# Performance work log

Hardware: AMD Instinct MI355X
Metric: run time of the kernel (lower is better)

Reference implementation:

```python
import jax, jax.numpy as jnp
import numpy as np

G = 128          # voxel grid extent: (range_max - range_min) / voxel_size
N = 100_000      # occupied input voxels (pre-unique)
CIN, COUT = 32, 64
BN_EPS = 1e-5


def _build_positions():
    rng = np.random.default_rng(0)
    pos = rng.integers(0, G, size=(N, 3), dtype=np.int32)
    pos = np.unique(pos, axis=0)  # one feature row per active voxel
    # calculate_grid: offsets (i-2) for i in 0..2 -> {-2,-1,0}^3, filter to [0,G), unique
    offs = np.stack(np.meshgrid(*([np.arange(-2, 1)] * 3), indexing='ij'), -1).reshape(-1, 3)
    op = (pos[:, None, :] + offs[None, :, :]).reshape(-1, 3)
    op = op[(op.min(1) >= 0) & (op.max(1) < G)]
    op = np.unique(op, axis=0)
    return pos.astype(np.int32), op.astype(np.int32)


def setup_inputs() -> dict:
    pos, out_pos = _build_positions()
    key = jax.random.key(0)
    kf, kw = jax.random.split(key)
    n_in = pos.shape[0]
    features = jax.random.normal(kf, (n_in, CIN), dtype=jnp.float32)
    # kaiming-style fan-in init for the 3x3x3 kernel: fan_in = 27 * CIN
    weight = jax.random.normal(kw, (27, CIN, COUT), dtype=jnp.float32) * np.float32(np.sqrt(2.0 / (27 * CIN)))
    gamma = jnp.ones((COUT,), jnp.float32)
    beta = jnp.zeros((COUT,), jnp.float32)
    return {"features": features, "weight": weight, "gamma": gamma, "beta": beta,
            "positions": jnp.asarray(pos), "out_positions": jnp.asarray(out_pos)}


def reference(features, weight, gamma, beta, positions, out_positions):
    n_in, cin = features.shape
    cout = weight.shape[-1]
    # dense coord -> row-index hash grid; pad by 2 since taps reach out_pos + 2
    grid = jnp.full((G + 2, G + 2, G + 2), -1, jnp.int32)
    grid = grid.at[positions[:, 0], positions[:, 1], positions[:, 2]].set(
        jnp.arange(n_in, dtype=jnp.int32))
    # row of zeros for missing neighbors (index -1 wraps to the last row)
    feat_pad = jnp.concatenate([features, jnp.zeros((1, cin), features.dtype)], axis=0)
    ox, oy, oz = out_positions[:, 0], out_positions[:, 1], out_positions[:, 2]
    out = jnp.zeros((out_positions.shape[0], cout), features.dtype)
    k = 0
    # out position o gathers inputs at o + {0,1,2}^3 (mirror of the {-2,-1,0} offsets)
    for dx in range(3):
        for dy in range(3):
            for dz in range(3):
                idx = grid[ox + dx, oy + dy, oz + dz]          # [M] (-1 if empty)
                out = out + feat_pad[idx] @ weight[k]          # [M,Cin]@[Cin,Cout]
                k += 1
    # BatchNorm1d (training mode, stats over all output voxels) + ReLU
    mean = out.mean(axis=0)
    var = out.var(axis=0)
    out = (out - mean) * jax.lax.rsqrt(var + BN_EPS) * gamma + beta
    return jax.nn.relu(out)
```

## Files before the change

kernel.cpp:

```cpp
#include <hip/hip_runtime.h>

#define GD 130
#define GD2 (GD*GD)
#define GRID_ELEMS (GD*GD*GD)
#define STATS_BYTES 1024
#define WPB 16
#define CONV_BLOCKS 256
#define MAX_NIN 100000
#define MAX_NOUT 1600000
#define WSTRIDE 5

typedef _Float16 f16x8 __attribute__((ext_vector_type(8)));
typedef float    f32x16 __attribute__((ext_vector_type(16)));

__device__ _Float16 g_feat16[(MAX_NIN + 1) * 32];
__device__ _Float16 g_out16[(size_t)MAX_NOUT * 64];

__device__ __forceinline__ f32x16 mfma_f16(uint4 a, uint4 b, f32x16 c) {
    union { uint4 u; f16x8 h; } A, B;
    A.u = a; B.u = b;
    return __builtin_amdgcn_mfma_f32_32x32x16_f16(A.h, B.h, c, 0, 0, 0);
}

__global__ __launch_bounds__(256) void scatter_grid_k(
    const int* __restrict__ pos, int* __restrict__ grid, int n_in)
{
    int i = blockIdx.x * blockDim.x + threadIdx.x;
    if (i < n_in) {
        int x = pos[3*i], y = pos[3*i+1], z = pos[3*i+2];
        grid[(x*GD + y)*GD + z] = i;
    }
}

__global__ __launch_bounds__(256) void feat_to_f16_k(
    const float* __restrict__ feat, int n_in)
{
    int i = (blockIdx.x * blockDim.x + threadIdx.x) * 8;
    const int ntot = (n_in + 1) * 32;
    if (i < ntot) {
        union { _Float16 h[8]; uint4 u; } t;
        if (i < n_in * 32) {
            const float4 a = *reinterpret_cast<const float4*>(feat + i);
            const float4 b = *reinterpret_cast<const float4*>(feat + i + 4);
            t.h[0] = (_Float16)a.x; t.h[1] = (_Float16)a.y;
            t.h[2] = (_Float16)a.z; t.h[3] = (_Float16)a.w;
            t.h[4] = (_Float16)b.x; t.h[5] = (_Float16)b.y;
            t.h[6] = (_Float16)b.z; t.h[7] = (_Float16)b.w;
        } else {
            t.u = uint4{0u, 0u, 0u, 0u};
        }
        *reinterpret_cast<uint4*>(g_feat16 + i) = t.u;
    }
}

__device__ __forceinline__ int4 probe4(const int* __restrict__ grid, int base) {
    int4 p;
    __builtin_memcpy(&p, grid + base, 16);
    return p;
}

__device__ __forceinline__ int sel3(int4 p, int dz) {
    return dz == 0 ? p.x : (dz == 1 ? p.y : p.z);
}

__global__ __launch_bounds__(1024) void conv_mfma_k(
    const float* __restrict__ W,
    const int* __restrict__ outpos, const int* __restrict__ grid,
    float* __restrict__ stats, int n_out, int n_in)
{
    __shared__ uint4 wlds[27*64*WSTRIDE];
    __shared__ float sstat[128];

    const int tid  = threadIdx.x;
    const int lane = tid & 63;
    const int wid  = tid >> 6;
    const int oc   = lane & 31;
    const int hi   = lane >> 5;

    for (int g = tid; g < 27*64*4; g += 1024) {
        const int k   = g >> 8;
        const int rem = g & 255;
        const int o   = rem >> 2;
        const int q   = rem & 3;
        union { _Float16 h[8]; uint4 u; } t;
        #pragma unroll
        for (int j = 0; j < 8; ++j)
            t.h[j] = (_Float16)W[k*2048 + (q*8 + j)*64 + o];
        wlds[(k*64 + o)*WSTRIDE + q] = t.u;
    }
    if (tid < 128) sstat[tid] = 0.f;
    __syncthreads();

    unsigned* g_o32 = reinterpret_cast<unsigned*>(g_out16);

    const int nchunks = (n_out + 63) >> 6;
    const int xcd  = blockIdx.x & 7;
    const int lw   = (blockIdx.x >> 3) * WPB + wid;
    const int nlw  = (gridDim.x >> 3) * WPB;
    const int Q    = (nchunks + 7) >> 3;
    const int cLo  = xcd * Q;
    const int cHi  = min(cLo + Q, nchunks);

    float ssum0 = 0.f, ssq0 = 0.f, ssum1 = 0.f, ssq1 = 0.f;

    for (int ch = cLo + lw; ch < cHi; ch += nlw) {
        const int r0 = ch << 6;
        const int rb0 = min(r0 + oc,      n_out - 1);
        const int rb1 = min(r0 + 32 + oc, n_out - 1);
        int3 c0, c1;
        __builtin_memcpy(&c0, outpos + 3*rb0, 12);
        __builtin_memcpy(&c1, outpos + 3*rb1, 12);
        const int gb0 = (c0.x*GD + c0.y)*GD + c0.z;
        const int gb1 = (c1.x*GD + c1.y)*GD + c1.z;

        f32x16 acc00 = {0.f};
        f32x16 acc01 = {0.f};
        f32x16 acc10 = {0.f};
        f32x16 acc11 = {0.f};

        #pragma unroll
        for (int g = 0; g < 9; ++g) {
            const int off = (g/3)*GD2 + (g%3)*GD;
            const int4 p0 = probe4(grid, gb0 + off);
            const int4 p1 = probe4(grid, gb1 + off);
            #pragma unroll
            for (int dz = 0; dz < 3; ++dz) {
                const int t = g*3 + dz;
                const int wb = (t*64 + oc)*WSTRIDE + hi;
                const uint4 b00 = wlds[wb];
                const uint4 b10 = wlds[wb + 2];
                const uint4 b01 = wlds[wb + 32*WSTRIDE];
                const uint4 b11 = wlds[wb + 32*WSTRIDE + 2];
                const int i0 = sel3(p0, dz);
                const int i1 = sel3(p1, dz);
                const int s0 = i0 < 0 ? n_in : i0;
                const int s1 = i1 < 0 ? n_in : i1;
                const uint4* fp0 = reinterpret_cast<const uint4*>(
                    g_feat16 + (size_t)s0 * 32);
                const uint4* fp1 = reinterpret_cast<const uint4*>(
                    g_feat16 + (size_t)s1 * 32);
                const uint4 a00 = fp0[hi], a01 = fp0[2 + hi];
                const uint4 a10 = fp1[hi], a11 = fp1[2 + hi];
                acc00 = mfma_f16(a00, b00, acc00);
                acc00 = mfma_f16(a01, b10, acc00);
                acc01 = mfma_f16(a00, b01, acc01);
                acc01 = mfma_f16(a01, b11, acc01);
                acc10 = mfma_f16(a10, b00, acc10);
                acc10 = mfma_f16(a11, b10, acc10);
                acc11 = mfma_f16(a10, b01, acc11);
                acc11 = mfma_f16(a11, b11, acc11);
            }
        }

        if (r0 + 64 <= n_out) {
            #pragma unroll
            for (int j = 0; j < 16; ++j) {
                const int rl = (j & 3) + 8*(j >> 2) + 4*hi;
                union { unsigned u; _Float16 h[2]; } q0, q1;
                const float v00 = acc00[j], v01 = acc01[j];
                const float v10 = acc10[j], v11 = acc11[j];
                q0.h[0] = (_Float16)v00; q0.h[1] = (_Float16)v01;
                q1.h[0] = (_Float16)v10; q1.h[1] = (_Float16)v11;
                g_o32[(size_t)(r0 + rl) * 32 + oc]      = q0.u;
                g_o32[(size_t)(r0 + 32 + rl) * 32 + oc] = q1.u;
                ssum0 += v00 + v10; ssq0 = fmaf(v00, v00, fmaf(v10, v10, ssq0));
                ssum1 += v01 + v11; ssq1 = fmaf(v01, v01, fmaf(v11, v11, ssq1));
            }
        } else {
            #pragma unroll
            for (int j = 0; j < 16; ++j) {
                const int rl = (j & 3) + 8*(j >> 2) + 4*hi;
                if (r0 + rl < n_out) {
                    const float v00 = acc00[j], v01 = acc01[j];
                    union { unsigned u; _Float16 h[2]; } q0;
                    q0.h[0] = (_Float16)v00; q0.h[1] = (_Float16)v01;
                    g_o32[(size_t)(r0 + rl) * 32 + oc] = q0.u;
                    ssum0 += v00; ssq0 = fmaf(v00, v00, ssq0);
                    ssum1 += v01; ssq1 = fmaf(v01, v01, ssq1);
                }
                if (r0 + 32 + rl < n_out) {
                    const float v10 = acc10[j], v11 = acc11[j];
                    union { unsigned u; _Float16 h[2]; } q1;
                    q1.h[0] = (_Float16)v10; q1.h[1] = (_Float16)v11;
                    g_o32[(size_t)(r0 + 32 + rl) * 32 + oc] = q1.u;
                    ssum0 += v10; ssq0 = fmaf(v10, v10, ssq0);
                    ssum1 += v11; ssq1 = fmaf(v11, v11, ssq1);
                }
            }
        }
    }

    atomicAdd(&sstat[oc],          ssum0);
    atomicAdd(&sstat[32 + oc],     ssum1);
    atomicAdd(&sstat[64 + oc],     ssq0);
    atomicAdd(&sstat[96 + oc],     ssq1);
    __syncthreads();
    if (tid < 128) unsafeAtomicAdd(&stats[tid], sstat[tid]);
}

__global__ __launch_bounds__(256) void bn_relu_k(
    float* __restrict__ out, const float* __restrict__ stats,
    const float* __restrict__ gamma, const float* __restrict__ beta, int n_out)
{
    __shared__ float sc[64], sh[64];
    if (threadIdx.x < 64) {
        const int c = threadIdx.x;
        const double inv_n = 1.0 / (double)n_out;
        const double mean = (double)stats[c] * inv_n;
        const double var  = (double)stats[64 + c] * inv_n - mean * mean;
        const float scale = gamma[c] * rsqrtf((float)var + 1e-5f);
        sc[c] = scale;
        sh[c] = beta[c] - (float)mean * scale;
    }
    __syncthreads();

    const size_t total8 = (size_t)n_out * 8;
    for (size_t t = (size_t)blockIdx.x * blockDim.x + threadIdx.x;
         t < total8; t += (size_t)gridDim.x * blockDim.x) {
        union { uint4 u; _Float16 h[8]; } v;
        v.u = *reinterpret_cast<const uint4*>(g_out16 + t * 8);
        const int c0 = ((int)(t & 7)) * 4;
        float4 r0, r1;
        r0.x = fmaxf(fmaf((float)v.h[0], sc[c0+0],    sh[c0+0]),    0.f);
        r1.x = fmaxf(fmaf((float)v.h[1], sc[c0+32],   sh[c0+32]),   0.f);
        r0.y = fmaxf(fmaf((float)v.h[2], sc[c0+1],    sh[c0+1]),    0.f);
        r1.y = fmaxf(fmaf((float)v.h[3], sc[c0+33],   sh[c0+33]),   0.f);
        r0.z = fmaxf(fmaf((float)v.h[4], sc[c0+2],    sh[c0+2]),    0.f);
        r1.z = fmaxf(fmaf((float)v.h[5], sc[c0+34],   sh[c0+34]),   0.f);
        r0.w = fmaxf(fmaf((float)v.h[6], sc[c0+3],    sh[c0+3]),    0.f);
        r1.w = fmaxf(fmaf((float)v.h[7], sc[c0+35],   sh[c0+35]),   0.f);
        float* rowp = out + (size_t)(t >> 3) * 64;
        *reinterpret_cast<float4*>(rowp + c0)      = r0;
        *reinterpret_cast<float4*>(rowp + 32 + c0) = r1;
    }
}

extern "C" void kernel_launch(void* const* d_in, const int* in_sizes, int n_in_arrs,
                              void* d_out, int out_size, void* d_ws, size_t ws_size,
                              hipStream_t stream)
{
    const float* feat   = (const float*)d_in[0];
    const float* W      = (const float*)d_in[1];
    const float* gamma  = (const float*)d_in[2];
    const float* beta   = (const float*)d_in[3];
    const int*   pos    = (const int*)d_in[4];
    const int*   outpos = (const int*)d_in[5];

    const int n_in  = in_sizes[0] / 32;
    const int n_out = in_sizes[5] / 3;

    float* out   = (float*)d_out;
    float* stats = (float*)d_ws;
    int*   grid  = (int*)((char*)d_ws + STATS_BYTES);

    hipMemsetAsync(stats, 0, STATS_BYTES, stream);
    hipMemsetAsync(grid, 0xFF, ((size_t)GRID_ELEMS + 4) * 4, stream);

    scatter_grid_k<<<(n_in + 255) / 256, 256, 0, stream>>>(pos, grid, n_in);
    feat_to_f16_k<<<((n_in + 1) * 4 + 255) / 256, 256, 0, stream>>>(feat, n_in);
    conv_mfma_k<<<CONV_BLOCKS, 1024, 0, stream>>>(W, outpos, grid, stats, n_out, n_in);
    bn_relu_k<<<2048, 256, 0, stream>>>(out, stats, gamma, beta, n_out);
}
```

Before: 369.0 us.

## Pre-convert weights to f16 in global memory and read them via cache instead of LDS

Adds a small kernel that converts the 27x32x64 weights to f16 once into a global buffer. The conv kernel drops its per-block LDS weight staging and instead loads the weight fragments straight from global memory, relying on the L1/L2 caches. This removes each block's redundant conversion prologue and the large LDS allocation, which frees occupancy, and the block count is doubled to use it. In exchange, every MFMA step now issues global/cache loads for weights where it used to read LDS, which may add latency in the inner loop.

```diff
diff --git a/kernel.cpp b/kernel.cpp
--- a/kernel.cpp
+++ b/kernel.cpp
@@ -5,16 +5,16 @@
 #define GRID_ELEMS (GD*GD*GD)
 #define STATS_BYTES 1024
 #define WPB 16
-#define CONV_BLOCKS 256
+#define CONV_BLOCKS 512
 #define MAX_NIN 100000
 #define MAX_NOUT 1600000
-#define WSTRIDE 5
 
 typedef _Float16 f16x8 __attribute__((ext_vector_type(8)));
 typedef float    f32x16 __attribute__((ext_vector_type(16)));
 
 __device__ _Float16 g_feat16[(MAX_NIN + 1) * 32];
 __device__ _Float16 g_out16[(size_t)MAX_NOUT * 64];
+__device__ uint4    g_w16[27 * 4 * 64];
 
 __device__ __forceinline__ f32x16 mfma_f16(uint4 a, uint4 b, f32x16 c) {
     union { uint4 u; f16x8 h; } A, B;
@@ -53,6 +53,21 @@
     }
 }
 
+__global__ __launch_bounds__(256) void w_to_f16_k(const float* __restrict__ W)
+{
+    int g = blockIdx.x * blockDim.x + threadIdx.x;
+    if (g < 27*4*64) {
+        const int k  = g >> 8;
+        const int kc = (g >> 6) & 3;
+        const int o  = g & 63;
+        union { _Float16 h[8]; uint4 u; } t;
+        #pragma unroll
+        for (int j = 0; j < 8; ++j)
+            t.h[j] = (_Float16)W[k*2048 + (kc*8 + j)*64 + o];
+        g_w16[g] = t.u;
+    }
+}
+
 __device__ __forceinline__ int4 probe4(const int* __restrict__ grid, int base) {
     int4 p;
     __builtin_memcpy(&p, grid + base, 16);
@@ -64,11 +79,9 @@
 }
 
 __global__ __launch_bounds__(1024) void conv_mfma_k(
-    const float* __restrict__ W,
     const int* __restrict__ outpos, const int* __restrict__ grid,
     float* __restrict__ stats, int n_out, int n_in)
 {
-    __shared__ uint4 wlds[27*64*WSTRIDE];
     __shared__ float sstat[128];
 
     const int tid  = threadIdx.x;
@@ -77,17 +90,6 @@
     const int oc   = lane & 31;
     const int hi   = lane >> 5;
 
-    for (int g = tid; g < 27*64*4; g += 1024) {
-        const int k   = g >> 8;
-        const int rem = g & 255;
-        const int o   = rem >> 2;
-        const int q   = rem & 3;
-        union { _Float16 h[8]; uint4 u; } t;
-        #pragma unroll
-        for (int j = 0; j < 8; ++j)
-            t.h[j] = (_Float16)W[k*2048 + (q*8 + j)*64 + o];
-        wlds[(k*64 + o)*WSTRIDE + q] = t.u;
-    }
     if (tid < 128) sstat[tid] = 0.f;
     __syncthreads();
 
@@ -126,11 +128,11 @@
             #pragma unroll
             for (int dz = 0; dz < 3; ++dz) {
                 const int t = g*3 + dz;
-                const int wb = (t*64 + oc)*WSTRIDE + hi;
-                const uint4 b00 = wlds[wb];
-                const uint4 b10 = wlds[wb + 2];
-                const uint4 b01 = wlds[wb + 32*WSTRIDE];
-                const uint4 b11 = wlds[wb + 32*WSTRIDE + 2];
+                const uint4* wt = g_w16 + t*256;
+                const uint4 b00 = wt[hi*64        + oc];
+                const uint4 b10 = wt[(2 + hi)*64  + oc];
+                const uint4 b01 = wt[hi*64        + 32 + oc];
+                const uint4 b11 = wt[(2 + hi)*64  + 32 + oc];
                 const int i0 = sel3(p0, dz);
                 const int i1 = sel3(p1, dz);
                 const int s0 = i0 < 0 ? n_in : i0;
@@ -258,6 +260,7 @@
 
     scatter_grid_k<<<(n_in + 255) / 256, 256, 0, stream>>>(pos, grid, n_in);
     feat_to_f16_k<<<((n_in + 1) * 4 + 255) / 256, 256, 0, stream>>>(feat, n_in);
-    conv_mfma_k<<<CONV_BLOCKS, 1024, 0, stream>>>(W, outpos, grid, stats, n_out, n_in);
+    w_to_f16_k<<<(27*4*64 + 255) / 256, 256, 0, stream>>>(W);
+    conv_mfma_k<<<CONV_BLOCKS, 1024, 0, stream>>>(outpos, grid, stats, n_out, n_in);
     bn_relu_k<<<2048, 256, 0, stream>>>(out, stats, gamma, beta, n_out);
 }
```

Result: slower. 598.6 us (+62.2%).

## Switch conv to 16x16x32 MFMA tiles with shuffled neighbor indices

Applied to the files above, without the earlier changes.

Replaces the 32x32x16 MFMA tiling with 16x16x32 MFMA over four 16-row groups and four 16-channel groups per 64-row chunk. Each lane now does one grid probe for a single output row and broadcasts neighbor indices with wave shuffles, halving the per-lane probe loads. Weights are laid out in LDS so each lane reads one contiguous uint4 per channel group, with no padding stride. Output writes use a new interleaved channel packing that must match the bn_relu reader, and 16 accumulator tiles plus shuffles raise register and instruction pressure.

```diff
diff --git a/kernel.cpp b/kernel.cpp
--- a/kernel.cpp
+++ b/kernel.cpp
@@ -8,18 +8,17 @@
 #define CONV_BLOCKS 256
 #define MAX_NIN 100000
 #define MAX_NOUT 1600000
-#define WSTRIDE 5
 
 typedef _Float16 f16x8 __attribute__((ext_vector_type(8)));
-typedef float    f32x16 __attribute__((ext_vector_type(16)));
+typedef float    f32x4 __attribute__((ext_vector_type(4)));
 
 __device__ _Float16 g_feat16[(MAX_NIN + 1) * 32];
 __device__ _Float16 g_out16[(size_t)MAX_NOUT * 64];
 
-__device__ __forceinline__ f32x16 mfma_f16(uint4 a, uint4 b, f32x16 c) {
+__device__ __forceinline__ f32x4 mfma16(uint4 a, uint4 b, f32x4 c) {
     union { uint4 u; f16x8 h; } A, B;
     A.u = a; B.u = b;
-    return __builtin_amdgcn_mfma_f32_32x32x16_f16(A.h, B.h, c, 0, 0, 0);
+    return __builtin_amdgcn_mfma_f32_16x16x32_f16(A.h, B.h, c, 0, 0, 0);
 }
 
 __global__ __launch_bounds__(256) void scatter_grid_k(
@@ -68,25 +67,27 @@
     const int* __restrict__ outpos, const int* __restrict__ grid,
     float* __restrict__ stats, int n_out, int n_in)
 {
-    __shared__ uint4 wlds[27*64*WSTRIDE];
+    __shared__ uint4 wlds[27*4*64];
     __shared__ float sstat[128];
 
     const int tid  = threadIdx.x;
     const int lane = tid & 63;
     const int wid  = tid >> 6;
-    const int oc   = lane & 31;
-    const int hi   = lane >> 5;
-
-    for (int g = tid; g < 27*64*4; g += 1024) {
-        const int k   = g >> 8;
+    const int lo   = lane & 15;
+    const int kc   = lane >> 4;
+
+    for (int g = tid; g < 27*4*64; g += 1024) {
+        const int t   = g >> 8;
         const int rem = g & 255;
-        const int o   = rem >> 2;
-        const int q   = rem & 3;
-        union { _Float16 h[8]; uint4 u; } t;
+        const int cg  = rem >> 6;
+        const int l   = rem & 63;
+        const int kcs = l >> 4;
+        const int co  = cg*16 + (l & 15);
+        union { _Float16 h[8]; uint4 u; } w;
         #pragma unroll
         for (int j = 0; j < 8; ++j)
-            t.h[j] = (_Float16)W[k*2048 + (q*8 + j)*64 + o];
-        wlds[(k*64 + o)*WSTRIDE + q] = t.u;
+            w.h[j] = (_Float16)W[t*2048 + (kcs*8 + j)*64 + co];
+        wlds[g] = w.u;
     }
     if (tid < 128) sstat[tid] = 0.f;
     __syncthreads();
@@ -101,99 +102,77 @@
     const int cLo  = xcd * Q;
     const int cHi  = min(cLo + Q, nchunks);
 
-    float ssum0 = 0.f, ssq0 = 0.f, ssum1 = 0.f, ssq1 = 0.f;
+    float ssum[4] = {0.f, 0.f, 0.f, 0.f};
+    float ssq[4]  = {0.f, 0.f, 0.f, 0.f};
 
     for (int ch = cLo + lw; ch < cHi; ch += nlw) {
         const int r0 = ch << 6;
-        const int rb0 = min(r0 + oc,      n_out - 1);
-        const int rb1 = min(r0 + 32 + oc, n_out - 1);
-        int3 c0, c1;
-        __builtin_memcpy(&c0, outpos + 3*rb0, 12);
-        __builtin_memcpy(&c1, outpos + 3*rb1, 12);
-        const int gb0 = (c0.x*GD + c0.y)*GD + c0.z;
-        const int gb1 = (c1.x*GD + c1.y)*GD + c1.z;
-
-        f32x16 acc00 = {0.f};
-        f32x16 acc01 = {0.f};
-        f32x16 acc10 = {0.f};
-        f32x16 acc11 = {0.f};
+        const int rb = min(r0 + lane, n_out - 1);
+        int3 c;
+        __builtin_memcpy(&c, outpos + 3*rb, 12);
+        const int gb = (c.x*GD + c.y)*GD + c.z;
+
+        f32x4 acc[4][4];
+        #pragma unroll
+        for (int rg = 0; rg < 4; ++rg)
+            #pragma unroll
+            for (int cg = 0; cg < 4; ++cg)
+                acc[rg][cg] = f32x4{0.f, 0.f, 0.f, 0.f};
 
         #pragma unroll
         for (int g = 0; g < 9; ++g) {
             const int off = (g/3)*GD2 + (g%3)*GD;
-            const int4 p0 = probe4(grid, gb0 + off);
-            const int4 p1 = probe4(grid, gb1 + off);
+            const int4 p = probe4(grid, gb + off);
             #pragma unroll
             for (int dz = 0; dz < 3; ++dz) {
                 const int t = g*3 + dz;
-                const int wb = (t*64 + oc)*WSTRIDE + hi;
-                const uint4 b00 = wlds[wb];
-                const uint4 b10 = wlds[wb + 2];
-                const uint4 b01 = wlds[wb + 32*WSTRIDE];
-                const uint4 b11 = wlds[wb + 32*WSTRIDE + 2];
-                const int i0 = sel3(p0, dz);
-                const int i1 = sel3(p1, dz);
-                const int s0 = i0 < 0 ? n_in : i0;
-                const int s1 = i1 < 0 ? n_in : i1;
-                const uint4* fp0 = reinterpret_cast<const uint4*>(
-                    g_feat16 + (size_t)s0 * 32);
-                const uint4* fp1 = reinterpret_cast<const uint4*>(
-                    g_feat16 + (size_t)s1 * 32);
-                const uint4 a00 = fp0[hi], a01 = fp0[2 + hi];
-                const uint4 a10 = fp1[hi], a11 = fp1[2 + hi];
-                acc00 = mfma_f16(a00, b00, acc00);
-                acc00 = mfma_f16(a01, b10, acc00);
-                acc01 = mfma_f16(a00, b01, acc01);
-                acc01 = mfma_f16(a01, b11, acc01);
-                acc10 = mfma_f16(a10, b00, acc10);
-                acc10 = mfma_f16(a11, b10, acc10);
-                acc11 = mfma_f16(a10, b01, acc11);
-                acc11 = mfma_f16(a11, b11, acc11);
-            }
-        }
-
-        if (r0 + 64 <= n_out) {
-            #pragma unroll
-            for (int j = 0; j < 16; ++j) {
-                const int rl = (j & 3) + 8*(j >> 2) + 4*hi;
-                union { unsigned u; _Float16 h[2]; } q0, q1;
-                const float v00 = acc00[j], v01 = acc01[j];
-                const float v10 = acc10[j], v11 = acc11[j];
-                q0.h[0] = (_Float16)v00; q0.h[1] = (_Float16)v01;
-                q1.h[0] = (_Float16)v10; q1.h[1] = (_Float16)v11;
-                g_o32[(size_t)(r0 + rl) * 32 + oc]      = q0.u;
-                g_o32[(size_t)(r0 + 32 + rl) * 32 + oc] = q1.u;
-                ssum0 += v00 + v10; ssq0 = fmaf(v00, v00, fmaf(v10, v10, ssq0));
-                ssum1 += v01 + v11; ssq1 = fmaf(v01, v01, fmaf(v11, v11, ssq1));
-            }
-        } else {
-            #pragma unroll
-            for (int j = 0; j < 16; ++j) {
-                const int rl = (j & 3) + 8*(j >> 2) + 4*hi;
-                if (r0 + rl < n_out) {
-                    const float v00 = acc00[j], v01 = acc01[j];
-                    union { unsigned u; _Float16 h[2]; } q0;
-                    q0.h[0] = (_Float16)v00; q0.h[1] = (_Float16)v01;
-                    g_o32[(size_t)(r0 + rl) * 32 + oc] = q0.u;
-                    ssum0 += v00; ssq0 = fmaf(v00, v00, ssq0);
-                    ssum1 += v01; ssq1 = fmaf(v01, v01, ssq1);
-                }
-                if (r0 + 32 + rl < n_out) {
-                    const float v10 = acc10[j], v11 = acc11[j];
-                    union { unsigned u; _Float16 h[2]; } q1;
-                    q1.h[0] = (_Float16)v10; q1.h[1] = (_Float16)v11;
-                    g_o32[(size_t)(r0 + 32 + rl) * 32 + oc] = q1.u;
-                    ssum0 += v10; ssq0 = fmaf(v10, v10, ssq0);
-                    ssum1 += v11; ssq1 = fmaf(v11, v11, ssq1);
+                const uint4 b0 = wlds[(t*4 + 0)*64 + lane];
+                const uint4 b1 = wlds[(t*4 + 1)*64 + lane];
+                const uint4 b2 = wlds[(t*4 + 2)*64 + lane];
+                const uint4 b3 = wlds[(t*4 + 3)*64 + lane];
+                const int v = sel3(p, dz);
+                #pragma unroll
+                for (int rg = 0; rg < 4; ++rg) {
+                    const int idx = __shfl(v, lo + 16*rg, 64);
+                    const int s = idx < 0 ? n_in : idx;
+                    const uint4 a = *reinterpret_cast<const uint4*>(
+                        g_feat16 + (size_t)s * 32 + kc * 8);
+                    acc[rg][0] = mfma16(a, b0, acc[rg][0]);
+                    acc[rg][1] = mfma16(a, b1, acc[rg][1]);
+                    acc[rg][2] = mfma16(a, b2, acc[rg][2]);
+                    acc[rg][3] = mfma16(a, b3, acc[rg][3]);
                 }
             }
         }
-    }
-
-    atomicAdd(&sstat[oc],          ssum0);
-    atomicAdd(&sstat[32 + oc],     ssum1);
-    atomicAdd(&sstat[64 + oc],     ssq0);
-    atomicAdd(&sstat[96 + oc],     ssq1);
+
+        const bool full = (r0 + 64 <= n_out);
+        #pragma unroll
+        for (int rg = 0; rg < 4; ++rg) {
+            #pragma unroll
+            for (int j = 0; j < 4; ++j) {
+                const int row = r0 + rg*16 + kc*4 + j;
+                if (full || row < n_out) {
+                    const float v0 = acc[rg][0][j], v1 = acc[rg][1][j];
+                    const float v2 = acc[rg][2][j], v3 = acc[rg][3][j];
+                    union { unsigned u; _Float16 h[2]; } q0, q1;
+                    q0.h[0] = (_Float16)v0; q0.h[1] = (_Float16)v2;
+                    q1.h[0] = (_Float16)v1; q1.h[1] = (_Float16)v3;
+                    g_o32[(size_t)row * 32 + lo]      = q0.u;
+                    g_o32[(size_t)row * 32 + 16 + lo] = q1.u;
+                    ssum[0] += v0; ssq[0] = fmaf(v0, v0, ssq[0]);
+                    ssum[1] += v1; ssq[1] = fmaf(v1, v1, ssq[1]);
+                    ssum[2] += v2; ssq[2] = fmaf(v2, v2, ssq[2]);
+                    ssum[3] += v3; ssq[3] = fmaf(v3, v3, ssq[3]);
+                }
+            }
+        }
+    }
+
+    #pragma unroll
+    for (int cg = 0; cg < 4; ++cg) {
+        atomicAdd(&sstat[cg*16 + lo],      ssum[cg]);
+        atomicAdd(&sstat[64 + cg*16 + lo], ssq[cg]);
+    }
     __syncthreads();
     if (tid < 128) unsafeAtomicAdd(&stats[tid], sstat[tid]);
 }
```

New measurement: 984.6 us. 167% more time.
